# Performance work log

Measured on AMD Instinct MI355X. Metric: run time of the kernel, lower is better.

## Reference

```python
import math
import jax, jax.numpy as jnp
import numpy as np

B, T, D, N = 4, 4096, 2048, 512
FACIL_RATE = 2.0
FIRE_THRESH = 0.85
MAX_GATE = 8.0
EPS = 1e-12  # F.normalize eps


def _gelu(x):
    c = math.sqrt(2.0 / math.pi)
    return 0.5 * x * (1.0 + jnp.tanh(c * (x + 0.044715 * x ** 3)))


def _normalize(v, axis=-1):
    n = jnp.linalg.norm(v, axis=axis, keepdims=True)
    return v / jnp.maximum(n, EPS)


def setup_inputs() -> dict:
    key = jax.random.key(0)
    k1, k2, k3 = jax.random.split(key, 3)
    return {
        "x": jax.random.normal(k1, (B, T, D), dtype=jnp.float32),
        "log_k_mag": jnp.asarray(math.log(0.5), dtype=jnp.float32),
        "keys": jax.random.normal(k2, (N, D), dtype=jnp.float32),
        "mag": jax.random.uniform(k3, (N, D), dtype=jnp.float32, minval=0.1, maxval=1.0),
        "facil": jnp.full((N,), 2.0, dtype=jnp.float32),
        "mask": jnp.ones((N,), dtype=bool),
    }


def reference(x, log_k_mag, keys, mag, facil, mask):
    Bb, Tt, Dd = x.shape
    k_mag = jnp.clip(jnp.exp(log_k_mag), 0.01, 5.0)
    y = _gelu(x)  # [B,T,D]
    # torch detaches y before the buffer math
    y_flat = jax.lax.stop_gradient(y.reshape(Bb * Tt, Dd))
    y_mean = y_flat.mean(0)  # [D]
    m_n = _normalize(y_mean, axis=0)
    keys_n = _normalize(keys)  # [N,D]
    sims = jnp.where(mask, keys_n @ m_n, -1.0)  # [N]
    idx = jnp.argmax(sims)
    fire = sims[idx] > FIRE_THRESH
    facil_level = jnp.where(fire, facil[idx] * FACIL_RATE, facil[idx])
    mag_vec = mag[idx]  # [D]
    importance = mag_vec / jnp.maximum(mag_vec.mean(), 1e-6)
    mv_n = keys_n[idx]  # [D] (already L2-normalized key)
    y_n = _normalize(y_flat)  # [B*T, D]
    tok_sim = jnp.clip(y_n @ mv_n, 0.0, 1.0).reshape(Bb, Tt, 1)
    gate_d = jnp.minimum(1.0 + k_mag * (facil_level - 1.0) * importance, MAX_GATE)  # [D]
    gate = gate_d.reshape(1, 1, Dd) * tok_sim + (1.0 - tok_sim)
    return y * gate
```

## Files before the change

### kernel.cpp

```cpp
#include <hip/hip_runtime.h>
#include <math.h>

#define ROWS 16384
#define D    2048
#define NKEYS 512
#define PBLK 2048
#define RPB  (ROWS / PBLK)

__device__ inline float gelu1(float v) {
    float t = 0.7978845608028654f * fmaf(0.044715f * v, v * v, v);
    float e = __expf(2.0f * t);
    return v * (1.0f - 1.0f / (e + 1.0f));
}

__device__ inline float4 gelu4(float4 v) {
    float4 r;
    r.x = gelu1(v.x); r.y = gelu1(v.y); r.z = gelu1(v.z); r.w = gelu1(v.w);
    return r;
}

__device__ inline void acc4(float4& a, float4 v) {
    a.x += v.x; a.y += v.y; a.z += v.z; a.w += v.w;
}

__device__ inline void block_reduce_sum2(float& a, float& b) {
    __shared__ float sa[4], sb[4];
    for (int off = 32; off; off >>= 1) {
        a += __shfl_down(a, off, 64);
        b += __shfl_down(b, off, 64);
    }
    const int lane = threadIdx.x & 63, w = threadIdx.x >> 6;
    if (lane == 0) { sa[w] = a; sb[w] = b; }
    __syncthreads();
    if (threadIdx.x == 0) {
        a = sa[0] + sa[1] + sa[2] + sa[3];
        b = sb[0] + sb[1] + sb[2] + sb[3];
        sa[0] = a; sb[0] = b;
    }
    __syncthreads();
    a = sa[0]; b = sb[0];
    __syncthreads();
}

__global__ __launch_bounds__(256) void colsum_kernel(const float* __restrict__ x,
                                                     float* __restrict__ partials) {
    const int t = threadIdx.x;
    const float4* xb = (const float4*)(x + (size_t)blockIdx.x * RPB * D);
    float4 a0 = {0.f,0.f,0.f,0.f}, a1 = {0.f,0.f,0.f,0.f};
    #pragma unroll
    for (int r = 0; r < RPB; r += 4) {
        const int b = r * (D / 4);
        float4 v0 = xb[b + 0*(D/4) + t];
        float4 w0 = xb[b + 0*(D/4) + t + 256];
        float4 v1 = xb[b + 1*(D/4) + t];
        float4 w1 = xb[b + 1*(D/4) + t + 256];
        float4 v2 = xb[b + 2*(D/4) + t];
        float4 w2 = xb[b + 2*(D/4) + t + 256];
        float4 v3 = xb[b + 3*(D/4) + t];
        float4 w3 = xb[b + 3*(D/4) + t + 256];
        acc4(a0, gelu4(v0)); acc4(a1, gelu4(w0));
        acc4(a0, gelu4(v1)); acc4(a1, gelu4(w1));
        acc4(a0, gelu4(v2)); acc4(a1, gelu4(w2));
        acc4(a0, gelu4(v3)); acc4(a1, gelu4(w3));
    }
    float4* pr = (float4*)(partials + (size_t)blockIdx.x * D);
    pr[t]       = a0;
    pr[t + 256] = a1;
}

__global__ __launch_bounds__(256) void reduce_kernel(const float* __restrict__ partials,
                                                     float* __restrict__ colsum) {
    const int t = threadIdx.x;
    const int cidx = t & 15;
    const int rg   = t >> 4;
    const int c = blockIdx.x * 16 + cidx;
    float s = 0.f;
    #pragma unroll 8
    for (int r = rg; r < PBLK; r += 16) {
        s += partials[(size_t)r * D + c];
    }
    __shared__ float sm[256];
    sm[t] = s;
    __syncthreads();
    if (t < 16) {
        float acc = 0.f;
        #pragma unroll
        for (int k = 0; k < 16; ++k) acc += sm[t + 16 * k];
        colsum[blockIdx.x * 16 + t] = acc;
    }
}

__global__ __launch_bounds__(256) void sims_kernel(const float* __restrict__ keys,
                                                   const float* __restrict__ colsum,
                                                   float* __restrict__ sims) {
    const int i = blockIdx.x;
    const int t = threadIdx.x;
    const float4* kr = (const float4*)(keys + (size_t)i * D);
    const float4* s4 = (const float4*)colsum;
    float4 k0 = kr[t], k1 = kr[t + 256];
    float4 c0 = s4[t], c1 = s4[t + 256];
    float dot = k0.x*c0.x + k0.y*c0.y + k0.z*c0.z + k0.w*c0.w
              + k1.x*c1.x + k1.y*c1.y + k1.z*c1.z + k1.w*c1.w;
    float ksq = k0.x*k0.x + k0.y*k0.y + k0.z*k0.z + k0.w*k0.w
              + k1.x*k1.x + k1.y*k1.y + k1.z*k1.z + k1.w*k1.w;
    block_reduce_sum2(dot, ksq);
    if (t == 0) sims[i] = dot / fmaxf(sqrtf(ksq), 1e-12f);
}

__global__ __launch_bounds__(256) void finalize_kernel(const float* __restrict__ colsum,
                                                       const float* __restrict__ sims,
                                                       const float* __restrict__ keys,
                                                       const float* __restrict__ mag,
                                                       const float* __restrict__ facil,
                                                       const float* __restrict__ logk,
                                                       float* __restrict__ gate_d,
                                                       float* __restrict__ mv_n) {
    const int t = threadIdx.x;
    __shared__ float sv[256];
    __shared__ int   si[256];
    __shared__ int   s_idx;
    __shared__ float s_val;

    float best = -3.402823466e38f; int bidx = 0;
    for (int i = t; i < NKEYS; i += 256) {
        float v = sims[i];
        if (v > best) { best = v; bidx = i; }
    }
    sv[t] = best; si[t] = bidx;
    __syncthreads();
    if (t == 0) {
        float bv = sv[0]; int bi = si[0];
        for (int i = 1; i < 256; i++) {
            if (sv[i] > bv || (sv[i] == bv && si[i] < bi)) { bv = sv[i]; bi = si[i]; }
        }
        s_idx = bi; s_val = bv;
    }
    __syncthreads();
    const int idx = s_idx;

    float ss = 0.f, dummy = 0.f;
    for (int d = t; d < D; d += 256) { float v = colsum[d]; ss += v * v; }
    block_reduce_sum2(ss, dummy);
    const float normS = fmaxf(sqrtf(ss), 1e-12f);
    const float true_sim = s_val / normS;
    const bool fire = true_sim > 0.85f;

    const float fl = facil[idx] * (fire ? 2.0f : 1.0f);
    const float km = fminf(fmaxf(expf(logk[0]), 0.01f), 5.0f);

    const float4* mrow4 = (const float4*)(mag  + (size_t)idx * D);
    const float4* krow4 = (const float4*)(keys + (size_t)idx * D);
    float4 mA = mrow4[t], mB = mrow4[t + 256];
    float4 kA = krow4[t], kB = krow4[t + 256];
    float msum = mA.x + mA.y + mA.z + mA.w + mB.x + mB.y + mB.z + mB.w;
    float ksq  = kA.x*kA.x + kA.y*kA.y + kA.z*kA.z + kA.w*kA.w
               + kB.x*kB.x + kB.y*kB.y + kB.z*kB.z + kB.w*kB.w;
    block_reduce_sum2(msum, ksq);
    const float mmean = fmaxf(msum / (float)D, 1e-6f);
    const float knorm = fmaxf(sqrtf(ksq), 1e-12f);
    const float coef = km * (fl - 1.0f) / mmean;
    const float rkn = 1.0f / knorm;

    float4 gA, gB, nA, nB;
    gA.x = fminf(fmaf(coef, mA.x, 1.0f), 8.0f);
    gA.y = fminf(fmaf(coef, mA.y, 1.0f), 8.0f);
    gA.z = fminf(fmaf(coef, mA.z, 1.0f), 8.0f);
    gA.w = fminf(fmaf(coef, mA.w, 1.0f), 8.0f);
    gB.x = fminf(fmaf(coef, mB.x, 1.0f), 8.0f);
    gB.y = fminf(fmaf(coef, mB.y, 1.0f), 8.0f);
    gB.z = fminf(fmaf(coef, mB.z, 1.0f), 8.0f);
    gB.w = fminf(fmaf(coef, mB.w, 1.0f), 8.0f);
    nA.x = kA.x * rkn; nA.y = kA.y * rkn; nA.z = kA.z * rkn; nA.w = kA.w * rkn;
    nB.x = kB.x * rkn; nB.y = kB.y * rkn; nB.z = kB.z * rkn; nB.w = kB.w * rkn;

    float4* g4 = (float4*)gate_d;
    float4* n4 = (float4*)mv_n;
    g4[t]       = gA;
    g4[t + 256] = gB;
    n4[t]       = nA;
    n4[t + 256] = nB;
}

__global__ __launch_bounds__(256) void main_kernel(const float* __restrict__ x,
                                                   const float* __restrict__ gate_d,
                                                   const float* __restrict__ mv_n,
                                                   float* __restrict__ out) {
    const int row = blockIdx.x;
    const int t = threadIdx.x;
    const float4* xr = (const float4*)(x + (size_t)row * D);
    float4 y0 = gelu4(xr[t]);
    float4 y1 = gelu4(xr[t + 256]);

    const float4* mv4 = (const float4*)mv_n;
    float4 m0 = mv4[t], m1 = mv4[t + 256];

    float dot = y0.x*m0.x + y0.y*m0.y + y0.z*m0.z + y0.w*m0.w
              + y1.x*m1.x + y1.y*m1.y + y1.z*m1.z + y1.w*m1.w;
    float ss  = y0.x*y0.x + y0.y*y0.y + y0.z*y0.z + y0.w*y0.w
              + y1.x*y1.x + y1.y*y1.y + y1.z*y1.z + y1.w*y1.w;
    block_reduce_sum2(dot, ss);

    float ts = dot / fmaxf(sqrtf(ss), 1e-12f);
    ts = fminf(fmaxf(ts, 0.0f), 1.0f);
    const float omts = 1.0f - ts;

    const float4* g4 = (const float4*)gate_d;
    float4 g0 = g4[t], g1 = g4[t + 256];

    float4 o0, o1;
    o0.x = y0.x * fmaf(g0.x, ts, omts);
    o0.y = y0.y * fmaf(g0.y, ts, omts);
    o0.z = y0.z * fmaf(g0.z, ts, omts);
    o0.w = y0.w * fmaf(g0.w, ts, omts);
    o1.x = y1.x * fmaf(g1.x, ts, omts);
    o1.y = y1.y * fmaf(g1.y, ts, omts);
    o1.z = y1.z * fmaf(g1.z, ts, omts);
    o1.w = y1.w * fmaf(g1.w, ts, omts);

    float4* outr = (float4*)(out + (size_t)row * D);
    outr[t]       = o0;
    outr[t + 256] = o1;
}

extern "C" void kernel_launch(void* const* d_in, const int* in_sizes, int n_in,
                              void* d_out, int out_size, void* d_ws, size_t ws_size,
                              hipStream_t stream) {
    const float* x     = (const float*)d_in[0];
    const float* logk  = (const float*)d_in[1];
    const float* keys  = (const float*)d_in[2];
    const float* mag   = (const float*)d_in[3];
    const float* facil = (const float*)d_in[4];
    float* out = (float*)d_out;

    float* ws       = (float*)d_ws;
    float* colsum   = ws;
    float* sims     = ws + 2048;
    float* gate_d   = ws + 2560;
    float* mv_n     = ws + 4608;
    float* partials = ws + 6656;

    colsum_kernel  <<<PBLK, 256, 0, stream>>>(x, partials);
    reduce_kernel  <<<D / 16, 256, 0, stream>>>(partials, colsum);
    sims_kernel    <<<NKEYS, 256, 0, stream>>>(keys, colsum, sims);
    finalize_kernel<<<1, 256, 0, stream>>>(colsum, sims, keys, mag, facil, logk, gate_d, mv_n);
    main_kernel    <<<ROWS, 256, 0, stream>>>(x, gate_d, mv_n, out);
}
```

Before: 115.4 us.

## Split column-sum pass into row-chunk by column-panel blocks with shared-memory reduction

```diff
diff --git a/kernel.cpp b/kernel.cpp
--- a/kernel.cpp
+++ b/kernel.cpp
@@ -4,8 +4,10 @@
 #define ROWS 16384
 #define D    2048
 #define NKEYS 512
-#define PBLK 2048
-#define RPB  (ROWS / PBLK)
+#define NCHUNK 1024
+#define CROWS (ROWS / NCHUNK)
+#define NPANEL 8
+#define PCOLS (D / NPANEL)
 
 __device__ inline float gelu1(float v) {
     float t = 0.7978845608028654f * fmaf(0.044715f * v, v * v, v);
@@ -44,28 +46,35 @@
 
 __global__ __launch_bounds__(256) void colsum_kernel(const float* __restrict__ x,
                                                      float* __restrict__ partials) {
-    const int t = threadIdx.x;
-    const float4* xb = (const float4*)(x + (size_t)blockIdx.x * RPB * D);
-    float4 a0 = {0.f,0.f,0.f,0.f}, a1 = {0.f,0.f,0.f,0.f};
-    #pragma unroll
-    for (int r = 0; r < RPB; r += 4) {
-        const int b = r * (D / 4);
-        float4 v0 = xb[b + 0*(D/4) + t];
-        float4 w0 = xb[b + 0*(D/4) + t + 256];
-        float4 v1 = xb[b + 1*(D/4) + t];
-        float4 w1 = xb[b + 1*(D/4) + t + 256];
-        float4 v2 = xb[b + 2*(D/4) + t];
-        float4 w2 = xb[b + 2*(D/4) + t + 256];
-        float4 v3 = xb[b + 3*(D/4) + t];
-        float4 w3 = xb[b + 3*(D/4) + t + 256];
-        acc4(a0, gelu4(v0)); acc4(a1, gelu4(w0));
-        acc4(a0, gelu4(v1)); acc4(a1, gelu4(w1));
-        acc4(a0, gelu4(v2)); acc4(a1, gelu4(w2));
-        acc4(a0, gelu4(v3)); acc4(a1, gelu4(w3));
-    }
-    float4* pr = (float4*)(partials + (size_t)blockIdx.x * D);
-    pr[t]       = a0;
-    pr[t + 256] = a1;
+    const int rc = blockIdx.x >> 3;
+    const int p  = blockIdx.x & 7;
+    const int t  = threadIdx.x;
+    const int w    = t >> 6;
+    const int lane = t & 63;
+
+    const size_t base = (size_t)(rc * CROWS + w) * (D / 4) + p * (PCOLS / 4) + lane;
+    const float4* x4 = (const float4*)x;
+    float4 l0 = x4[base + 0 * 4 * (D / 4)];
+    float4 l1 = x4[base + 1 * 4 * (D / 4)];
+    float4 l2 = x4[base + 2 * 4 * (D / 4)];
+    float4 l3 = x4[base + 3 * 4 * (D / 4)];
+
+    float4 a = gelu4(l0);
+    acc4(a, gelu4(l1));
+    acc4(a, gelu4(l2));
+    acc4(a, gelu4(l3));
+
+    __shared__ float4 sm[4][64];
+    sm[w][lane] = a;
+    __syncthreads();
+    if (t < 64) {
+        float4 s = sm[0][t];
+        acc4(s, sm[1][t]);
+        acc4(s, sm[2][t]);
+        acc4(s, sm[3][t]);
+        float4* pr = (float4*)(partials + (size_t)rc * D + p * PCOLS);
+        pr[t] = s;
+    }
 }
 
 __global__ __launch_bounds__(256) void reduce_kernel(const float* __restrict__ partials,
@@ -76,7 +85,7 @@
     const int c = blockIdx.x * 16 + cidx;
     float s = 0.f;
     #pragma unroll 8
-    for (int r = rg; r < PBLK; r += 16) {
+    for (int r = rg; r < NCHUNK; r += 16) {
         s += partials[(size_t)r * D + c];
     }
     __shared__ float sm[256];
@@ -239,7 +248,7 @@
     float* mv_n     = ws + 4608;
     float* partials = ws + 6656;
 
-    colsum_kernel  <<<PBLK, 256, 0, stream>>>(x, partials);
+    colsum_kernel  <<<NCHUNK * NPANEL, 256, 0, stream>>>(x, partials);
     reduce_kernel  <<<D / 16, 256, 0, stream>>>(partials, colsum);
     sims_kernel    <<<NKEYS, 256, 0, stream>>>(keys, colsum, sims);
     finalize_kernel<<<1, 256, 0, stream>>>(colsum, sims, keys, mag, facil, logk, gate_d, mv_n);
```

After: 103.3 us. -10.5%, faster.
